# Optimization experiments

Measured on AMD Instinct MI355X. Metric: run time of the kernel, lower is better.

The kernel has to match this reference:

```python
import jax, jax.numpy as jnp
import numpy as np

SEQ, BATCH, IN_DIM, HID = 256, 1024, 512, 256  # hidden_dim == n_qubits (required by f*cx)


def setup_inputs() -> dict:
    key = jax.random.key(0)
    ks = jax.random.split(key, 14)
    comb = IN_DIM + HID
    lim = 1.0 / np.sqrt(comb)  # torch Linear default init scale
    def lin(kw, kb):
        W = jax.random.uniform(kw, (HID, comb), jnp.float32, -lim, lim)
        b = jax.random.uniform(kb, (HID,), jnp.float32, -lim, lim)
        return W, b
    Wf, bf = lin(ks[0], ks[1])
    Wi, bi = lin(ks[2], ks[3])
    Wu, bu = lin(ks[4], ks[5])
    Wo, bo = lin(ks[6], ks[7])
    # QLayer params ~ np.random.randn(n_wires)
    pf = jax.random.normal(ks[8], (HID,), jnp.float32)
    pi = jax.random.normal(ks[9], (HID,), jnp.float32)
    pu = jax.random.normal(ks[10], (HID,), jnp.float32)
    po = jax.random.normal(ks[11], (HID,), jnp.float32)
    inputs = jax.random.normal(ks[12], (SEQ, BATCH, IN_DIM), jnp.float32)
    return {"inputs": inputs, "Wf": Wf, "bf": bf, "Wi": Wi, "bi": bi,
            "Wu": Wu, "bu": bu, "Wo": Wo, "bo": bo,
            "pf": pf, "pi": pi, "pu": pu, "po": po}


def _qlayer(z, p):
    # Analytic form of the PennyLane circuit: RX(z_j)RX(p_j) per wire, CNOT ladder,
    # PauliZ expvals  =>  <Z_k> = prod_{j<=k} cos(z_j + p_j)
    return jnp.cumprod(jnp.cos(z + p), axis=-1)


def reference(inputs, Wf, bf, Wi, bi, Wu, bu, Wo, bo, pf, pi, pu, po):
    B = inputs.shape[1]
    h0 = jnp.zeros((B, HID), inputs.dtype)
    c0 = jnp.zeros((B, HID), inputs.dtype)

    def step(carry, x):
        hx, cx = carry
        comb = jnp.concatenate([x, hx], axis=1)            # [B, IN+HID]
        f = jax.nn.sigmoid(_qlayer(comb @ Wf.T + bf, pf))  # [B, HID]
        i = jax.nn.sigmoid(_qlayer(comb @ Wi.T + bi, pi))
        g = jnp.tanh(_qlayer(comb @ Wu.T + bu, pu))
        o = jax.nn.sigmoid(_qlayer(comb @ Wo.T + bo, po))
        cx = f * cx + i * g
        hx = o * jnp.tanh(cx)
        return (hx, cx), hx

    (hx, cx), outs = jax.lax.scan(step, (h0, c0), inputs)
    return outs, (hx, cx)
```

## Files before the change

kernel.cpp:

```cpp
#include <hip/hip_runtime.h>
#include <stdint.h>
#include <math.h>

#define SEQ 256
#define BATCH 1024
#define IN_DIM 512
#define HID 256
#define NCOL 1024

typedef float f32x4 __attribute__((ext_vector_type(4)));
typedef float f32x16 __attribute__((ext_vector_type(16)));
typedef short bf16x8 __attribute__((ext_vector_type(8)));
typedef int i32x4 __attribute__((ext_vector_type(4)));
typedef int i32x16 __attribute__((ext_vector_type(16)));
typedef unsigned short u16;

#define QS_W 3519.5272410266f
#define DEQ  (1.0f / (16129.0f * 27.712812921102035f))
#define INV2PI 0.15915494309189535f
#define DEQREV (DEQ * INV2PI)

__device__ __forceinline__ u16 f2b(float f) {
  union { float f; uint32_t u; } v; v.f = f;
  uint32_t r = v.u + 0x7FFFu + ((v.u >> 16) & 1u);
  return (u16)(r >> 16);
}
__device__ __forceinline__ float b2f(uint32_t h16) {
  union { uint32_t u; float f; } v; v.u = h16 << 16;
  return v.f;
}

#define LOG2E 1.4426950408889634f
__device__ __forceinline__ float fsig(float x) {
  return __builtin_amdgcn_rcpf(1.0f + __builtin_amdgcn_exp2f(-x * LOG2E));
}
__device__ __forceinline__ float ftanh(float x) {
  float e = __builtin_amdgcn_exp2f(x * (2.0f * LOG2E));
  return (e - 1.0f) * __builtin_amdgcn_rcpf(e + 1.0f);
}
__device__ __forceinline__ void barrier_lds_only() {
  asm volatile("s_waitcnt lgkmcnt(0)\n\ts_barrier" ::: "memory");
}
template <int CTRL, int RM>
__device__ __forceinline__ float dpp_mul_step(float p) {
  int t = __builtin_amdgcn_update_dpp(
      __builtin_bit_cast(int, 1.0f), __builtin_bit_cast(int, p),
      CTRL, RM, 0xf, false);
  return p * __builtin_bit_cast(float, t);
}
__device__ __forceinline__ float wave_scan_mul(float p) {
  p = dpp_mul_step<0x111, 0xf>(p);
  p = dpp_mul_step<0x112, 0xf>(p);
  p = dpp_mul_step<0x114, 0xf>(p);
  p = dpp_mul_step<0x118, 0xf>(p);
  p = dpp_mul_step<0x142, 0xa>(p);
  p = dpp_mul_step<0x143, 0xc>(p);
  return p;
}
__device__ __forceinline__ float wave_shr1_one(float p) {
  int t = __builtin_amdgcn_update_dpp(
      __builtin_bit_cast(int, 1.0f), __builtin_bit_cast(int, p),
      0x138, 0xf, 0xf, false);
  return __builtin_bit_cast(float, t);
}

__global__ __launch_bounds__(256) void qlstm_prep(
    const float* __restrict__ Wf, const float* __restrict__ Wi,
    const float* __restrict__ Wu, const float* __restrict__ Wo,
    const float* __restrict__ bf_, const float* __restrict__ bi_,
    const float* __restrict__ bu_, const float* __restrict__ bo_,
    const float* __restrict__ pf_, const float* __restrict__ pi_,
    const float* __restrict__ pu_, const float* __restrict__ po_,
    u16* __restrict__ Wxb32, signed char* __restrict__ Whb32,
    float* __restrict__ bp_all) {
  int idx = blockIdx.x * 256 + threadIdx.x;
  if (idx >= NCOL * 768) return;
  int n = idx / 768, k = idx - n * 768;
  int g = n >> 8, nn = n & 255;
  const float* W = (g == 0) ? Wf : (g == 1) ? Wi : (g == 2) ? Wu : Wo;
  float wv = W[nn * 768 + k];
  if (k == 0) {
    float bb = (g == 0 ? bf_ : g == 1 ? bi_ : g == 2 ? bu_ : bo_)[nn];
    float pp = (g == 0 ? pf_ : g == 1 ? pi_ : g == 2 ? pu_ : po_)[nn];
    bp_all[n] = bb + pp;
  }
  if (k < IN_DIM) {
    int nt32 = n >> 5, kb = k >> 4, hi = (k >> 3) & 1, e = k & 7;
    int lane_ = (n & 31) + 32 * hi;
    Wxb32[(((size_t)(nt32 * 32 + kb) * 64 + lane_) << 3) + e] = f2b(wv);
  } else {
    int kh = k - IN_DIM;
    int ks = kh >> 5;
    int hi = (kh >> 4) & 1;
    int e = kh & 15;
    int lane_ = (n & 31) + 32 * hi;
    int q = (int)rintf(wv * QS_W);
    Whb32[(((size_t)((n >> 5) * 8 + ks) * 64 + lane_) << 4) + e] = (signed char)q;
  }
}

__global__ __launch_bounds__(512, 1) void qlstm_k1(
    const float* __restrict__ Xc, const u16* __restrict__ Wxb32,
    u16* __restrict__ Zxf) {
  __shared__ uint4 A_lds[128 * 64];
  int bid = blockIdx.x;
  size_t m0 = (size_t)bid * 128;
  int tid = threadIdx.x, lane = tid & 63, w = tid >> 6;
  int rh = w & 1, cg = w >> 1;

#pragma unroll
  for (int i = 0; i < 16; ++i) {
    int tt = w * 16 + i;
    int row = ((tt >> 5) << 5) + (lane & 31);
    int k0 = ((tt & 31) * 2 + (lane >> 5)) * 8;
    const float* xp = Xc + (m0 + row) * IN_DIM + k0;
    float4 xa = *(const float4*)xp;
    float4 xb = *(const float4*)(xp + 4);
    uint4 pk;
    pk.x = (uint32_t)f2b(xa.x * INV2PI) | ((uint32_t)f2b(xa.y * INV2PI) << 16);
    pk.y = (uint32_t)f2b(xa.z * INV2PI) | ((uint32_t)f2b(xa.w * INV2PI) << 16);
    pk.z = (uint32_t)f2b(xb.x * INV2PI) | ((uint32_t)f2b(xb.y * INV2PI) << 16);
    pk.w = (uint32_t)f2b(xb.z * INV2PI) | ((uint32_t)f2b(xb.w * INV2PI) << 16);
    A_lds[tt * 64 + lane] = pk;
  }
  __syncthreads();

  const f32x16 zero16 = {0.f, 0.f, 0.f, 0.f, 0.f, 0.f, 0.f, 0.f,
                         0.f, 0.f, 0.f, 0.f, 0.f, 0.f, 0.f, 0.f};
  for (int ntbp = 0; ntbp < 4; ++ntbp) {
    f32x16 acc[2][2];
    acc[0][0] = zero16; acc[0][1] = zero16;
    acc[1][0] = zero16; acc[1][1] = zero16;
    int nt0 = (2 * ntbp + 0) * 4 + cg;
    int nt1 = (2 * ntbp + 1) * 4 + cg;
#pragma unroll 8
    for (int kb = 0; kb < 32; ++kb) {
      bf16x8 a0 = *(const bf16x8*)&A_lds[((rh * 2 + 0) * 32 + kb) * 64 + lane];
      bf16x8 a1 = *(const bf16x8*)&A_lds[((rh * 2 + 1) * 32 + kb) * 64 + lane];
      bf16x8 b0 = *(const bf16x8*)(Wxb32 + (((size_t)(nt0 * 32 + kb) * 64 + lane) << 3));
      bf16x8 b1 = *(const bf16x8*)(Wxb32 + (((size_t)(nt1 * 32 + kb) * 64 + lane) << 3));
      acc[0][0] = __builtin_amdgcn_mfma_f32_32x32x16_bf16(a0, b0, acc[0][0], 0, 0, 0);
      acc[0][1] = __builtin_amdgcn_mfma_f32_32x32x16_bf16(a1, b0, acc[0][1], 0, 0, 0);
      acc[1][0] = __builtin_amdgcn_mfma_f32_32x32x16_bf16(a0, b1, acc[1][0], 0, 0, 0);
      acc[1][1] = __builtin_amdgcn_mfma_f32_32x32x16_bf16(a1, b1, acc[1][1], 0, 0, 0);
    }
#pragma unroll
    for (int q = 0; q < 2; ++q) {
      int nt32 = (q == 0) ? nt0 : nt1;
#pragma unroll
      for (int sf = 0; sf < 2; ++sf) {
#pragma unroll
        for (int rq = 0; rq < 4; ++rq) {
          uint2 pk;
          pk.x = (uint32_t)f2b(acc[q][sf][rq * 4 + 0]) |
                 ((uint32_t)f2b(acc[q][sf][rq * 4 + 1]) << 16);
          pk.y = (uint32_t)f2b(acc[q][sf][rq * 4 + 2]) |
                 ((uint32_t)f2b(acc[q][sf][rq * 4 + 3]) << 16);
          size_t rb8 = (size_t)bid * 16 + rh * 8 + sf * 4 + rq;
          *(uint2*)(Zxf + (rb8 * 32 + nt32) * 256 + lane * 4) = pk;
        }
      }
    }
  }
}

__global__ __launch_bounds__(512, 2) void qlstm_k2(
    const u16* __restrict__ Zxf, const signed char* __restrict__ Whb32,
    const float* __restrict__ bp_all,
    float* __restrict__ h_state, float* __restrict__ c_state,
    float* __restrict__ outp, int t0, int Tc) {
  __shared__ float z_lds[8][1300];
  __shared__ uint4 wres[6144];
  __shared__ uint4 h8q[512];

  int tid = threadIdx.x, lane = tid & 63, w = tid >> 6;
  int rg = blockIdx.x;
  int r0 = rg * 8;

  h8q[tid] = (uint4){0, 0, 0, 0};
  for (int u = tid; u < 6144; u += 512) {
    int nt = u >> 7, rem = u & 127;
    int ks = rem >> 6, ln = rem & 63;
    wres[u] = *(const uint4*)(Whb32 + (((size_t)(nt * 8 + ks) * 64 + ln) << 4));
  }
  int col0 = lane * 4;
  float ca[4], hp[4];
  {
    float4 c4 = *(const float4*)(c_state + (size_t)(r0 + w) * HID + col0);
    float4 h4 = *(const float4*)(h_state + (size_t)(r0 + w) * HID + col0);
    ca[0] = c4.x; ca[1] = c4.y; ca[2] = c4.z; ca[3] = c4.w;
    hp[0] = h4.x; hp[1] = h4.y; hp[2] = h4.z; hp[3] = h4.w;
    uint32_t pk = 0;
#pragma unroll
    for (int j = 0; j < 4; ++j) {
      int q = (int)rintf(hp[j] * 127.f);
      pk |= ((uint32_t)(q & 255)) << (8 * j);
    }
    ((uint32_t*)h8q)[w * 64 + (((col0) ^ ((w & 7) << 4)) >> 2)] = pk;
  }
  __syncthreads();

  float bp4r[4];
#pragma unroll
  for (int j = 0; j < 4; ++j)
    bp4r[j] = bp_all[(w * 4 + j) * 32 + (lane & 31)];

#define AFR(ks) (*(const i32x4*)((const char*)h8q + \
    (((lane & 31) << 8) + (((((ks) << 5)) + ((lane >> 5) << 4)) ^ ((lane & 7) << 4)))))
#define BRES(j, ks) (*(const i32x4*)&wres[(((w * 4 + (j)) * 3 + (ks)) << 6) + lane])
  const signed char* wsb = Whb32 + ((size_t)(w * 4) << 13) + ((size_t)lane << 4);
#define LDWS(j, ks) (*(const i32x4*)(wsb + ((j) << 13) + ((ks) << 10)))

  const u16* zb = Zxf + ((size_t)rg * 32 + w * 4) * 256 + lane * 4;
  const size_t ZT = (size_t)128 * 32 * 256;
  uint2 zc[4], zn[4];
#pragma unroll
  for (int j = 0; j < 4; ++j) zc[j] = *(const uint2*)(zb + (size_t)j * 256);
  i32x4 s3[4], s4[4], s5[4], s6[4], s7[4];
#pragma unroll
  for (int j = 0; j < 4; ++j) s3[j] = LDWS(j, 3);
#pragma unroll
  for (int j = 0; j < 4; ++j) s4[j] = LDWS(j, 4);
#pragma unroll
  for (int j = 0; j < 4; ++j) s5[j] = LDWS(j, 5);
#pragma unroll
  for (int j = 0; j < 4; ++j) s6[j] = LDWS(j, 6);
#pragma unroll
  for (int j = 0; j < 4; ++j) s7[j] = LDWS(j, 7);
  const i32x16 z16 = {0, 0, 0, 0, 0, 0, 0, 0, 0, 0, 0, 0, 0, 0, 0, 0};

  for (int tt = 0; tt < Tc; ++tt) {
    i32x16 acc[4];
    i32x4 a;
    a = AFR(0);
#pragma unroll
    for (int j = 0; j < 4; ++j)
      acc[j] = __builtin_amdgcn_mfma_i32_32x32x32_i8(a, BRES(j, 0), z16, 0, 0, 0);
    a = AFR(1);
#pragma unroll
    for (int j = 0; j < 4; ++j)
      acc[j] = __builtin_amdgcn_mfma_i32_32x32x32_i8(a, BRES(j, 1), acc[j], 0, 0, 0);
    a = AFR(2);
#pragma unroll
    for (int j = 0; j < 4; ++j)
      acc[j] = __builtin_amdgcn_mfma_i32_32x32x32_i8(a, BRES(j, 2), acc[j], 0, 0, 0);
    a = AFR(3);
#pragma unroll
    for (int j = 0; j < 4; ++j)
      acc[j] = __builtin_amdgcn_mfma_i32_32x32x32_i8(a, s3[j], acc[j], 0, 0, 0);
#pragma unroll
    for (int j = 0; j < 4; ++j) s3[j] = LDWS(j, 3);
    a = AFR(4);
#pragma unroll
    for (int j = 0; j < 4; ++j)
      acc[j] = __builtin_amdgcn_mfma_i32_32x32x32_i8(a, s4[j], acc[j], 0, 0, 0);
#pragma unroll
    for (int j = 0; j < 4; ++j) s4[j] = LDWS(j, 4);
    a = AFR(5);
#pragma unroll
    for (int j = 0; j < 4; ++j)
      acc[j] = __builtin_amdgcn_mfma_i32_32x32x32_i8(a, s5[j], acc[j], 0, 0, 0);
#pragma unroll
    for (int j = 0; j < 4; ++j) s5[j] = LDWS(j, 5);
    a = AFR(6);
#pragma unroll
    for (int j = 0; j < 4; ++j)
      acc[j] = __builtin_amdgcn_mfma_i32_32x32x32_i8(a, s6[j], acc[j], 0, 0, 0);
#pragma unroll
    for (int j = 0; j < 4; ++j) s6[j] = LDWS(j, 6);
    a = AFR(7);
#pragma unroll
    for (int j = 0; j < 4; ++j)
      acc[j] = __builtin_amdgcn_mfma_i32_32x32x32_i8(a, s7[j], acc[j], 0, 0, 0);
#pragma unroll
    for (int j = 0; j < 4; ++j) s7[j] = LDWS(j, 7);
    {
      size_t tnext = (size_t)((tt + 1 < Tc) ? tt + 1 : tt) * ZT;
#pragma unroll
      for (int j = 0; j < 4; ++j)
        zn[j] = *(const uint2*)(zb + tnext + (size_t)j * 256);
    }
    int rb = 4 * (lane >> 5);
#pragma unroll
    for (int j = 0; j < 4; ++j) {
      int colw = (w * 4 + j) * 32 + (lane & 31);
      float bpj = bp4r[j];
      float z0 = b2f(zc[j].x & 0xffffu) + bpj * INV2PI;
      float z1 = b2f(zc[j].x >> 16) + bpj * INV2PI;
      float z2 = b2f(zc[j].y & 0xffffu) + bpj * INV2PI;
      float z3 = b2f(zc[j].y >> 16) + bpj * INV2PI;
      z_lds[rb + 0][colw] = __builtin_amdgcn_cosf((float)acc[j][0] * DEQREV + z0);
      z_lds[rb + 1][colw] = __builtin_amdgcn_cosf((float)acc[j][1] * DEQREV + z1);
      z_lds[rb + 2][colw] = __builtin_amdgcn_cosf((float)acc[j][2] * DEQREV + z2);
      z_lds[rb + 3][colw] = __builtin_amdgcn_cosf((float)acc[j][3] * DEQREV + z3);
    }
    barrier_lds_only();
    float4 v0 = *(const float4*)&z_lds[w][0 * 256 + col0];
    float4 v1 = *(const float4*)&z_lds[w][1 * 256 + col0];
    float4 v2 = *(const float4*)&z_lds[w][2 * 256 + col0];
    float4 v3 = *(const float4*)&z_lds[w][3 * 256 + col0];
    float p0 = wave_scan_mul(v0.x * v0.y * v0.z * v0.w);
    float p1 = wave_scan_mul(v1.x * v1.y * v1.z * v1.w);
    float p2 = wave_scan_mul(v2.x * v2.y * v2.z * v2.w);
    float p3 = wave_scan_mul(v3.x * v3.y * v3.z * v3.w);
    float e0 = wave_shr1_one(p0), e1 = wave_shr1_one(p1);
    float e2 = wave_shr1_one(p2), e3 = wave_shr1_one(p3);
    float q0[4], q1[4], q2[4], q3[4];
    q0[0] = e0 * v0.x; q0[1] = q0[0] * v0.y; q0[2] = q0[1] * v0.z; q0[3] = q0[2] * v0.w;
    q1[0] = e1 * v1.x; q1[1] = q1[0] * v1.y; q1[2] = q1[1] * v1.z; q1[3] = q1[2] * v1.w;
    q2[0] = e2 * v2.x; q2[1] = q2[0] * v2.y; q2[2] = q2[1] * v2.z; q2[3] = q2[2] * v2.w;
    q3[0] = e3 * v3.x; q3[1] = q3[0] * v3.y; q3[2] = q3[1] * v3.z; q3[3] = q3[2] * v3.w;
    uint32_t pk = 0;
#pragma unroll
    for (int j = 0; j < 4; ++j) {
      float fg = fsig(q0[j]);
      float ig = fsig(q1[j]);
      float ug = ftanh(q2[j]);
      float og = fsig(q3[j]);
      ca[j] = fg * ca[j] + ig * ug;
      float hv = og * ftanh(ca[j]);
      hp[j] = hv;
      int q = (int)rintf(hv * 127.f);
      pk |= ((uint32_t)(q & 255)) << (8 * j);
    }
    ((uint32_t*)h8q)[w * 64 + (((col0) ^ ((w & 7) << 4)) >> 2)] = pk;
    {
      float4 h4;
      h4.x = hp[0]; h4.y = hp[1]; h4.z = hp[2]; h4.w = hp[3];
      *(float4*)(outp + ((size_t)(t0 + tt) * BATCH + r0 + w) * HID + col0) = h4;
    }
    barrier_lds_only();
#pragma unroll
    for (int j = 0; j < 4; ++j) zc[j] = zn[j];
  }
#undef AFR
#undef BRES
#undef LDWS
  {
    float4 h4, c4;
    h4.x = hp[0]; h4.y = hp[1]; h4.z = hp[2]; h4.w = hp[3];
    c4.x = ca[0]; c4.y = ca[1]; c4.z = ca[2]; c4.w = ca[3];
    *(float4*)(h_state + (size_t)(r0 + w) * HID + col0) = h4;
    *(float4*)(c_state + (size_t)(r0 + w) * HID + col0) = c4;
    if (t0 + Tc == SEQ) {
      size_t base = (size_t)SEQ * BATCH * HID;
      *(float4*)(outp + base + (size_t)(r0 + w) * HID + col0) = h4;
      *(float4*)(outp + base + (size_t)BATCH * HID + (size_t)(r0 + w) * HID + col0) = c4;
    }
  }
}

extern "C" void kernel_launch(void* const* d_in, const int* in_sizes, int n_in,
                              void* d_out, int out_size, void* d_ws, size_t ws_size,
                              hipStream_t stream) {
  const float* X  = (const float*)d_in[0];
  const float* Wf = (const float*)d_in[1];
  const float* bf_ = (const float*)d_in[2];
  const float* Wi = (const float*)d_in[3];
  const float* bi_ = (const float*)d_in[4];
  const float* Wu = (const float*)d_in[5];
  const float* bu_ = (const float*)d_in[6];
  const float* Wo = (const float*)d_in[7];
  const float* bo_ = (const float*)d_in[8];
  const float* pf_ = (const float*)d_in[9];
  const float* pi_ = (const float*)d_in[10];
  const float* pu_ = (const float*)d_in[11];
  const float* po_ = (const float*)d_in[12];

  char* ws = (char*)d_ws;
  signed char* Whb32 = (signed char*)ws;
  u16* Wxb32 = (u16*)(ws + (512 << 10));
  float* bp_all = (float*)(ws + (1536 << 10));
  float* h_state = (float*)(ws + (2048 << 10));
  float* c_state = (float*)(ws + (3072 << 10));
  u16* Zxf = (u16*)(ws + (4096 << 10));

  size_t fixed = (size_t)4096 << 10;
  int Tc = 256;
  while (Tc > 1 && fixed + (size_t)Tc * (2u << 20) > ws_size) Tc >>= 1;
  if (fixed + (size_t)Tc * (2u << 20) > ws_size) return;

  qlstm_prep<<<3072, 256, 0, stream>>>(Wf, Wi, Wu, Wo, bf_, bi_, bu_, bo_,
                                       pf_, pi_, pu_, po_, Wxb32, Whb32, bp_all);
  hipMemsetAsync(h_state, 0, 2u << 20, stream);

  for (int t0 = 0; t0 < SEQ; t0 += Tc) {
    qlstm_k1<<<dim3(Tc * 8), 512, 0, stream>>>(X + (size_t)t0 * BATCH * IN_DIM, Wxb32, Zxf);
    qlstm_k2<<<dim3(128), 512, 0, stream>>>(Zxf, Whb32, bp_all,
                                            h_state, c_state, (float*)d_out, t0, Tc);
  }
}
```

Measured before the change: 1.043 ms.

## Retile input GEMM to 64-row blocks, fold bias into Zx, polynomial sigmoid

```diff
diff --git a/kernel.cpp b/kernel.cpp
--- a/kernel.cpp
+++ b/kernel.cpp
@@ -31,8 +31,10 @@
 }
 
 #define LOG2E 1.4426950408889634f
-__device__ __forceinline__ float fsig(float x) {
-  return __builtin_amdgcn_rcpf(1.0f + __builtin_amdgcn_exp2f(-x * LOG2E));
+__device__ __forceinline__ float sigp(float x) {
+  float u = x * x;
+  float p = fmaf(u, fmaf(u, 0.00208333333f, -0.0208333333f), 0.25f);
+  return fmaf(x, p, 0.5f);
 }
 __device__ __forceinline__ float ftanh(float x) {
   float e = __builtin_amdgcn_exp2f(x * (2.0f * LOG2E));
@@ -99,20 +101,20 @@
   }
 }
 
-__global__ __launch_bounds__(512, 1) void qlstm_k1(
+__global__ __launch_bounds__(512, 4) void qlstm_k1(
     const float* __restrict__ Xc, const u16* __restrict__ Wxb32,
-    u16* __restrict__ Zxf) {
-  __shared__ uint4 A_lds[128 * 64];
+    const float* __restrict__ bp_all, u16* __restrict__ Zxf) {
+  __shared__ uint4 A_lds[64 * 64];
   int bid = blockIdx.x;
-  size_t m0 = (size_t)bid * 128;
+  size_t m0 = (size_t)bid * 64;
   int tid = threadIdx.x, lane = tid & 63, w = tid >> 6;
-  int rh = w & 1, cg = w >> 1;
-
-#pragma unroll
-  for (int i = 0; i < 16; ++i) {
-    int tt = w * 16 + i;
-    int row = ((tt >> 5) << 5) + (lane & 31);
-    int k0 = ((tt & 31) * 2 + (lane >> 5)) * 8;
+
+#pragma unroll
+  for (int i = 0; i < 8; ++i) {
+    int slot = i * 512 + tid;
+    int tt = slot >> 6, ln = slot & 63;
+    int row = ((tt >> 5) << 5) + (ln & 31);
+    int k0 = (tt & 31) * 16 + (ln >> 5) * 8;
     const float* xp = Xc + (m0 + row) * IN_DIM + k0;
     float4 xa = *(const float4*)xp;
     float4 xb = *(const float4*)(xp + 4);
@@ -121,52 +123,58 @@
     pk.y = (uint32_t)f2b(xa.z * INV2PI) | ((uint32_t)f2b(xa.w * INV2PI) << 16);
     pk.z = (uint32_t)f2b(xb.x * INV2PI) | ((uint32_t)f2b(xb.y * INV2PI) << 16);
     pk.w = (uint32_t)f2b(xb.z * INV2PI) | ((uint32_t)f2b(xb.w * INV2PI) << 16);
-    A_lds[tt * 64 + lane] = pk;
+    A_lds[slot] = pk;
   }
   __syncthreads();
 
   const f32x16 zero16 = {0.f, 0.f, 0.f, 0.f, 0.f, 0.f, 0.f, 0.f,
                          0.f, 0.f, 0.f, 0.f, 0.f, 0.f, 0.f, 0.f};
-  for (int ntbp = 0; ntbp < 4; ++ntbp) {
+#define LDB(nt, kb) (*(const bf16x8*)(Wxb32 + (((size_t)((nt) * 32 + (kb)) * 64 + lane) << 3)))
+  for (int p = 0; p < 2; ++p) {
     f32x16 acc[2][2];
     acc[0][0] = zero16; acc[0][1] = zero16;
     acc[1][0] = zero16; acc[1][1] = zero16;
-    int nt0 = (2 * ntbp + 0) * 4 + cg;
-    int nt1 = (2 * ntbp + 1) * 4 + cg;
+    int nt0 = w * 4 + 2 * p;
+    int nt1 = w * 4 + 2 * p + 1;
+    bf16x8 b0 = LDB(nt0, 0), b1 = LDB(nt1, 0);
 #pragma unroll 8
     for (int kb = 0; kb < 32; ++kb) {
-      bf16x8 a0 = *(const bf16x8*)&A_lds[((rh * 2 + 0) * 32 + kb) * 64 + lane];
-      bf16x8 a1 = *(const bf16x8*)&A_lds[((rh * 2 + 1) * 32 + kb) * 64 + lane];
-      bf16x8 b0 = *(const bf16x8*)(Wxb32 + (((size_t)(nt0 * 32 + kb) * 64 + lane) << 3));
-      bf16x8 b1 = *(const bf16x8*)(Wxb32 + (((size_t)(nt1 * 32 + kb) * 64 + lane) << 3));
+      bf16x8 a0 = *(const bf16x8*)&A_lds[(0 * 32 + kb) * 64 + lane];
+      bf16x8 a1 = *(const bf16x8*)&A_lds[(1 * 32 + kb) * 64 + lane];
+      bf16x8 nb0, nb1;
+      if (kb < 31) { nb0 = LDB(nt0, kb + 1); nb1 = LDB(nt1, kb + 1); }
       acc[0][0] = __builtin_amdgcn_mfma_f32_32x32x16_bf16(a0, b0, acc[0][0], 0, 0, 0);
       acc[0][1] = __builtin_amdgcn_mfma_f32_32x32x16_bf16(a1, b0, acc[0][1], 0, 0, 0);
       acc[1][0] = __builtin_amdgcn_mfma_f32_32x32x16_bf16(a0, b1, acc[1][0], 0, 0, 0);
       acc[1][1] = __builtin_amdgcn_mfma_f32_32x32x16_bf16(a1, b1, acc[1][1], 0, 0, 0);
-    }
+      if (kb < 31) { b0 = nb0; b1 = nb1; }
+    }
+    float bpv0 = bp_all[nt0 * 32 + (lane & 31)] * INV2PI;
+    float bpv1 = bp_all[nt1 * 32 + (lane & 31)] * INV2PI;
 #pragma unroll
     for (int q = 0; q < 2; ++q) {
       int nt32 = (q == 0) ? nt0 : nt1;
+      float bpv = (q == 0) ? bpv0 : bpv1;
 #pragma unroll
       for (int sf = 0; sf < 2; ++sf) {
 #pragma unroll
         for (int rq = 0; rq < 4; ++rq) {
           uint2 pk;
-          pk.x = (uint32_t)f2b(acc[q][sf][rq * 4 + 0]) |
-                 ((uint32_t)f2b(acc[q][sf][rq * 4 + 1]) << 16);
-          pk.y = (uint32_t)f2b(acc[q][sf][rq * 4 + 2]) |
-                 ((uint32_t)f2b(acc[q][sf][rq * 4 + 3]) << 16);
-          size_t rb8 = (size_t)bid * 16 + rh * 8 + sf * 4 + rq;
+          pk.x = (uint32_t)f2b(acc[q][sf][rq * 4 + 0] + bpv) |
+                 ((uint32_t)f2b(acc[q][sf][rq * 4 + 1] + bpv) << 16);
+          pk.y = (uint32_t)f2b(acc[q][sf][rq * 4 + 2] + bpv) |
+                 ((uint32_t)f2b(acc[q][sf][rq * 4 + 3] + bpv) << 16);
+          size_t rb8 = (size_t)bid * 8 + sf * 4 + rq;
           *(uint2*)(Zxf + (rb8 * 32 + nt32) * 256 + lane * 4) = pk;
         }
       }
     }
   }
+#undef LDB
 }
 
 __global__ __launch_bounds__(512, 2) void qlstm_k2(
     const u16* __restrict__ Zxf, const signed char* __restrict__ Whb32,
-    const float* __restrict__ bp_all,
     float* __restrict__ h_state, float* __restrict__ c_state,
     float* __restrict__ outp, int t0, int Tc) {
   __shared__ float z_lds[8][1300];
@@ -179,7 +187,7 @@
 
   h8q[tid] = (uint4){0, 0, 0, 0};
   for (int u = tid; u < 6144; u += 512) {
-    int nt = u >> 7, rem = u & 127;
+    int nt = u / 192, rem = u - nt * 192;
     int ks = rem >> 6, ln = rem & 63;
     wres[u] = *(const uint4*)(Whb32 + (((size_t)(nt * 8 + ks) * 64 + ln) << 4));
   }
@@ -200,11 +208,6 @@
   }
   __syncthreads();
 
-  float bp4r[4];
-#pragma unroll
-  for (int j = 0; j < 4; ++j)
-    bp4r[j] = bp_all[(w * 4 + j) * 32 + (lane & 31)];
-
 #define AFR(ks) (*(const i32x4*)((const char*)h8q + \
     (((lane & 31) << 8) + (((((ks) << 5)) + ((lane >> 5) << 4)) ^ ((lane & 7) << 4)))))
 #define BRES(j, ks) (*(const i32x4*)&wres[(((w * 4 + (j)) * 3 + (ks)) << 6) + lane])
@@ -284,15 +287,14 @@
 #pragma unroll
     for (int j = 0; j < 4; ++j) {
       int colw = (w * 4 + j) * 32 + (lane & 31);
-      float bpj = bp4r[j];
-      float z0 = b2f(zc[j].x & 0xffffu) + bpj * INV2PI;
-      float z1 = b2f(zc[j].x >> 16) + bpj * INV2PI;
-      float z2 = b2f(zc[j].y & 0xffffu) + bpj * INV2PI;
-      float z3 = b2f(zc[j].y >> 16) + bpj * INV2PI;
-      z_lds[rb + 0][colw] = __builtin_amdgcn_cosf((float)acc[j][0] * DEQREV + z0);
-      z_lds[rb + 1][colw] = __builtin_amdgcn_cosf((float)acc[j][1] * DEQREV + z1);
-      z_lds[rb + 2][colw] = __builtin_amdgcn_cosf((float)acc[j][2] * DEQREV + z2);
-      z_lds[rb + 3][colw] = __builtin_amdgcn_cosf((float)acc[j][3] * DEQREV + z3);
+      float z0 = b2f(zc[j].x & 0xffffu);
+      float z1 = b2f(zc[j].x >> 16);
+      float z2 = b2f(zc[j].y & 0xffffu);
+      float z3 = b2f(zc[j].y >> 16);
+      z_lds[rb + 0][colw] = __builtin_amdgcn_cosf(fmaf((float)acc[j][0], DEQREV, z0));
+      z_lds[rb + 1][colw] = __builtin_amdgcn_cosf(fmaf((float)acc[j][1], DEQREV, z1));
+      z_lds[rb + 2][colw] = __builtin_amdgcn_cosf(fmaf((float)acc[j][2], DEQREV, z2));
+      z_lds[rb + 3][colw] = __builtin_amdgcn_cosf(fmaf((float)acc[j][3], DEQREV, z3));
     }
     barrier_lds_only();
     float4 v0 = *(const float4*)&z_lds[w][0 * 256 + col0];
@@ -313,10 +315,10 @@
     uint32_t pk = 0;
 #pragma unroll
     for (int j = 0; j < 4; ++j) {
-      float fg = fsig(q0[j]);
-      float ig = fsig(q1[j]);
+      float fg = sigp(q0[j]);
+      float ig = sigp(q1[j]);
       float ug = ftanh(q2[j]);
-      float og = fsig(q3[j]);
+      float og = sigp(q3[j]);
       ca[j] = fg * ca[j] + ig * ug;
       float hv = og * ftanh(ca[j]);
       hp[j] = hv;
@@ -385,8 +387,9 @@
   hipMemsetAsync(h_state, 0, 2u << 20, stream);
 
   for (int t0 = 0; t0 < SEQ; t0 += Tc) {
-    qlstm_k1<<<dim3(Tc * 8), 512, 0, stream>>>(X + (size_t)t0 * BATCH * IN_DIM, Wxb32, Zxf);
-    qlstm_k2<<<dim3(128), 512, 0, stream>>>(Zxf, Whb32, bp_all,
+    qlstm_k1<<<dim3(Tc * 16), 512, 0, stream>>>(X + (size_t)t0 * BATCH * IN_DIM,
+                                                Wxb32, bp_all, Zxf);
+    qlstm_k2<<<dim3(128), 512, 0, stream>>>(Zxf, Whb32,
                                             h_state, c_state, (float*)d_out, t0, Tc);
   }
 }
```

After: 943.9 us. 1.11x faster.
